# Optimization experiments

Measured on AMD Instinct MI355X. Metric: run time of the kernel, lower is better.

Reference implementation:

```python
import jax, jax.numpy as jnp
import numpy as np

EPS = 1e-06
FP8_MAX = 448.0  # float8_e4m3fn max
T, H = 8192, 4096


def setup_inputs() -> dict:
    key = jax.random.key(0)
    ks = jax.random.split(key, 5)
    return {
        "hidden_states": jax.random.normal(ks[0], (T, H), dtype=jnp.float32),
        "norm_w": jax.random.uniform(ks[1], (4, H), dtype=jnp.float32),
        "w": jax.random.uniform(ks[2], (3, H, H), dtype=jnp.float32),
        "wscale": jax.random.uniform(ks[3], (3,), dtype=jnp.float32),
        "scale": jax.random.uniform(ks[4], (3,), dtype=jnp.float32),
    }


def _rmsnorm(x, g):
    var = jnp.mean(x * x, axis=-1, keepdims=True)
    return x * jax.lax.rsqrt(var + EPS) * g


def _fp8_quant(x, s):
    # static per-tensor quant: scale, clamp to fp8 range, cast to e4m3 and back
    q = jnp.clip(x / s, -FP8_MAX, FP8_MAX)
    return q.astype(jnp.float8_e4m3fn).astype(jnp.float32)


def _fp8_linear(x, wq, s_in, s_w):
    qx = _fp8_quant(x, s_in)
    return (qx @ wq) * (s_in * s_w)


def reference(hidden_states, norm_w, w, wscale, scale):
    # weight fp8 quantization (module stores weights already in fp8)
    wq = w.astype(jnp.float8_e4m3fn).astype(jnp.float32)  # [3,H,H]

    z = jax.nn.relu(hidden_states)
    x = resid = z  # all_reduce == identity on one device
    y = _rmsnorm(x, norm_w[0])

    z2 = _fp8_linear(y, wq[0], scale[0], wscale[0])
    x2 = z2 + resid
    resid = x2
    y2 = _rmsnorm(x2, norm_w[1])

    z3 = _fp8_linear(y2, wq[1], scale[1], wscale[1])
    x3 = z3 + resid
    resid = x3
    y3 = _rmsnorm(x3, norm_w[2])

    z4 = _fp8_linear(y3, wq[2], scale[2], wscale[2])
    x4 = z4 + resid
    y4 = _rmsnorm(x4, norm_w[3])
    return y4
```

## Files before the change

### kernel.cpp

```cpp
#include <hip/hip_runtime.h>

typedef float f32x4  __attribute__((ext_vector_type(4)));
typedef float f32x16 __attribute__((ext_vector_type(16)));
typedef int   i32x4  __attribute__((ext_vector_type(4)));
typedef int   i32x8  __attribute__((ext_vector_type(8)));

#define T_DIM 8192
#define H_DIM 4096
#define SC1 0x7f7f7f7f

__device__ __forceinline__ unsigned int pack_fp8x4(float a, float b, float c, float d) {
    int v = __builtin_amdgcn_cvt_pk_fp8_f32(a, b, 0, false);
    v = __builtin_amdgcn_cvt_pk_fp8_f32(c, d, v, true);
    return (unsigned int)v;
}


__global__ __launch_bounds__(256) void wquant_kernel(
    const float* __restrict__ w, unsigned char* __restrict__ wqT)
{
    const int l  = blockIdx.z;
    const int n0 = blockIdx.x * 64;
    const int k0 = blockIdx.y * 64;
    const int tid = threadIdx.x;
    __shared__ unsigned char tile[64][68];
    const float* wl = w + (size_t)l * H_DIM * H_DIM;
#pragma unroll
    for (int p = 0; p < 4; ++p) {
        int r = p * 16 + (tid >> 4);
        int c = (tid & 15) * 4;
        f32x4 v = *(const f32x4*)(wl + (size_t)(k0 + r) * H_DIM + n0 + c);
        *(unsigned int*)&tile[r][c] = pack_fp8x4(v[0], v[1], v[2], v[3]);
    }
    __syncthreads();
    const int nl = tid >> 2;
    const int g  = tid & 3;
    unsigned int words[4];
#pragma unroll
    for (int wi = 0; wi < 4; ++wi) {
        unsigned int a = 0;
#pragma unroll
        for (int b = 0; b < 4; ++b)
            a |= (unsigned int)tile[g * 16 + wi * 4 + b][nl] << (8 * b);
        words[wi] = a;
    }
    const int bn = n0 >> 8, wc = (n0 >> 6) & 3, kt = k0 >> 6;
    const int n2 = nl >> 5;
    const int lane = (g >> 1) * 32 + (nl & 31);
    const int byte0 = (g & 1) * 16;
    const size_t off = ((((size_t)l * 16 + bn) * 64 + kt) * 4 + wc) * 2 + n2;
    unsigned char* op = wqT + off * 2048 + lane * 32 + byte0;
    uint4 ov; ov.x = words[0]; ov.y = words[1]; ov.z = words[2]; ov.w = words[3];
    *(uint4*)op = ov;
}

template <int MODE>
__global__ __launch_bounds__(256) void row_kernel(
    const float* __restrict__ in,
    float* __restrict__ resid_out,
    void* __restrict__ out,
    const float* __restrict__ g,
    const float* __restrict__ scale_p)
{
    const int row = blockIdx.x;
    const int tid = threadIdx.x;
    const float* rin = in + (size_t)row * H_DIM;
    float x[16];
    float ss = 0.0f;
#pragma unroll
    for (int j = 0; j < 4; ++j) {
        const int base = (j * 256 + tid) * 4;
        f32x4 v = *(const f32x4*)(rin + base);
        f32x4 rv;
#pragma unroll
        for (int i = 0; i < 4; ++i) {
            float t = v[i];
            if (MODE == 0) t = fmaxf(t, 0.0f);
            x[j * 4 + i] = t;
            rv[i] = t;
            ss += t * t;
        }
        if (MODE == 0)
            *(f32x4*)(resid_out + (size_t)row * H_DIM + base) = rv;
    }
#pragma unroll
    for (int off = 32; off > 0; off >>= 1)
        ss += __shfl_down(ss, off, 64);
    __shared__ float red[4];
    if ((tid & 63) == 0) red[tid >> 6] = ss;
    __syncthreads();
    const float var  = (red[0] + red[1] + red[2] + red[3]) * (1.0f / (float)H_DIM);
    const float rinv = 1.0f / sqrtf(var + 1e-6f);

    if (MODE == 2) {
        float* ro = (float*)out + (size_t)row * H_DIM;
#pragma unroll
        for (int j = 0; j < 4; ++j) {
            const int base = (j * 256 + tid) * 4;
            f32x4 gv = *(const f32x4*)(g + base);
            f32x4 ov;
#pragma unroll
            for (int i = 0; i < 4; ++i) ov[i] = (x[j * 4 + i] * rinv) * gv[i];
            *(f32x4*)(ro + base) = ov;
        }
    } else {
        const float s = scale_p[0];
        unsigned int* qo = (unsigned int*)out + (size_t)row * (H_DIM / 4);
#pragma unroll
        for (int j = 0; j < 4; ++j) {
            const int base = (j * 256 + tid) * 4;
            f32x4 gv = *(const f32x4*)(g + base);
            float q[4];
#pragma unroll
            for (int i = 0; i < 4; ++i) {
                float y = (x[j * 4 + i] * rinv) * gv[i];
                y = y / s;
                q[i] = fminf(fmaxf(y, -448.0f), 448.0f);
            }
            qo[j * 256 + tid] = pack_fp8x4(q[0], q[1], q[2], q[3]);
        }
    }
}

__device__ __forceinline__ void stage_half(const unsigned char* gsrc, unsigned char* ldsdst) {
    __builtin_amdgcn_global_load_lds(
        (const __attribute__((address_space(1))) unsigned int*)gsrc,
        (__attribute__((address_space(3))) unsigned int*)ldsdst, 16, 0, 0);
}

#define VM8 asm volatile("s_waitcnt vmcnt(8)" ::: "memory")
#define VM4 asm volatile("s_waitcnt vmcnt(4)" ::: "memory")
#define VM0 asm volatile("s_waitcnt vmcnt(0)" ::: "memory")
#define BAR __builtin_amdgcn_s_barrier()
#define PRIO1 __builtin_amdgcn_s_setprio(1)
#define PRIO0 __builtin_amdgcn_s_setprio(0)

#define MM2(m, S) do {                                                          \
    acc[m][0] = __builtin_amdgcn_mfma_scale_f32_32x32x64_f8f6f4(                \
        fa[m], b##S##0, acc[m][0], 0, 0, 0, SC1, 0, SC1);                       \
    acc[m][1] = __builtin_amdgcn_mfma_scale_f32_32x32x64_f8f6f4(                \
        fa[m], b##S##1, acc[m][1], 0, 0, 0, SC1, 0, SC1);                       \
} while (0)

#define RDA(BUF, m) do {                                                        \
    *(i32x4*)&fa[m]         = *(const i32x4*)(lds + (BUF) + wrA + (m) * 2048 + fo0); \
    *(((i32x4*)&fa[m]) + 1) = *(const i32x4*)(lds + (BUF) + wrA + (m) * 2048 + fo1); \
} while (0)

#define TILEBODY(S, BR) do {                                                    \
    PRIO1; MM2(0, S); PRIO0; RDA(BR, 0);                                        \
    PRIO1; MM2(1, S); PRIO0; RDA(BR, 1);                                        \
    PRIO1; MM2(2, S); PRIO0; RDA(BR, 2);                                        \
    PRIO1; MM2(3, S); PRIO0; RDA(BR, 3);                                        \
    __builtin_amdgcn_sched_group_barrier(0x008, 4, 0);                          \
    __builtin_amdgcn_sched_group_barrier(0x100, 4, 0);                          \
    __builtin_amdgcn_sched_group_barrier(0x008, 4, 0);                          \
    __builtin_amdgcn_sched_group_barrier(0x100, 4, 0);                          \
} while (0)

#define TILELAST(S) do {                                                        \
    PRIO1; MM2(0, S); MM2(1, S); MM2(2, S); MM2(3, S); PRIO0;                   \
} while (0)

#define LDB(NX) do {                                                            \
    bE##NX##0 = *(const i32x8*)(gB0 + kb);                                      \
    bE##NX##1 = *(const i32x8*)(gB0 + kb + 2048);                               \
    bO##NX##0 = *(const i32x8*)(gB0 + kb + 16384);                              \
    bO##NX##1 = *(const i32x8*)(gB0 + kb + 16384 + 2048);                       \
    kb += 32768;                                                                \
} while (0)

#define STG(KOFF, BUF) do {                                                     \
    stage_half(gAlo + (KOFF), lds + (BUF) + wave * 1024);                       \
    stage_half(gAhi + (KOFF), lds + (BUF) + 8192 + wave * 1024);                \
} while (0)

#define ITER(CU, NX, BR1, BR2, BS1, BS2) do {                                   \
    LDB(NX);                                                                    \
    STG(ka, BS1); STG(ka + 64, BS2); ka += 128;                                 \
    VM8; BAR;                                                                   \
    TILEBODY(E##CU, BR1);                                                       \
    TILEBODY(O##CU, BR2);                                                       \
} while (0)

__global__ __launch_bounds__(512, 2) void gemm_fp8_kernel(
    const unsigned char* __restrict__ A,
    const unsigned char* __restrict__ B,
    float* __restrict__ C,
    const float* __restrict__ s_in,
    const float* __restrict__ s_w)
{
    __shared__ unsigned char lds[98304];

    const float alpha = s_in[0] * s_w[0];

    const int b = blockIdx.x;
    const int local = b >> 3, chunk = b & 7;
    const int bm = (chunk & 3) * 8 + (local & 7);
    const int bn = (chunk >> 2) * 8 + (local >> 3);

    const int tid  = threadIdx.x;
    const int wave = tid >> 6;
    const int lane = tid & 63;
    const int wr   = wave >> 2;
    const int wc   = wave & 3;

    const int sw  = (lane >> 1) & 3;
    const int fo0 = (lane & 31) * 64 + ((((lane >> 5) * 2) + 0 ^ sw)) * 16;
    const int fo1 = (lane & 31) * 64 + ((((lane >> 5) * 2) + 1 ^ sw)) * 16;
    const int wrA = wr * 8192;

    const int voff = (tid >> 2) * H_DIM + ((tid & 3) ^ ((tid >> 3) & 3)) * 16;
    const unsigned char* gAlo = A + (size_t)bm * 256 * H_DIM + voff;
    const unsigned char* gAhi = gAlo + (size_t)128 * H_DIM;

    const unsigned char* gB0 =
        B + ((((size_t)bn * 64) * 4 + wc) * 2) * 2048 + lane * 32;

    f32x16 acc[4][2];
#pragma unroll
    for (int m = 0; m < 4; ++m)
#pragma unroll
        for (int n = 0; n < 2; ++n)
#pragma unroll
            for (int e = 0; e < 16; ++e) acc[m][n][e] = 0.0f;

    i32x8 fa[4];
    i32x8 bEA0, bEA1, bOA0, bOA1, bEB0, bEB1, bOB0, bOB1;
    int ka, kb;

    STG(0,   0);
    STG(64,  16384);
    STG(128, 32768);
    STG(192, 49152);
    kb = 0; LDB(A);
    VM0; BAR;
    RDA(0, 0); RDA(0, 1); RDA(0, 2); RDA(0, 3);
    ka = 256;

#pragma unroll 1
    for (int it = 0; it < 5; ++it) {
        ITER(A, B, 16384, 32768, 65536, 81920);
        ITER(B, A, 49152, 65536, 0,     16384);
        ITER(A, B, 81920, 0,     32768, 49152);
        ITER(B, A, 16384, 32768, 65536, 81920);
        ITER(A, B, 49152, 65536, 0,     16384);
        ITER(B, A, 81920, 0,     32768, 49152);
    }
    LDB(B);
    VM4; BAR;
    TILEBODY(EA, 16384);
    TILEBODY(OA, 32768);
    VM0; BAR;
    TILEBODY(EB, 49152);
    TILELAST(OB);

    const int lrow0 = bm * 256 + wr * 128 + 4 * (lane >> 5);
    const int lcol0 = bn * 256 + wc * 64 + (lane & 31);
#pragma unroll
    for (int m = 0; m < 4; ++m) {
#pragma unroll
        for (int n = 0; n < 2; ++n) {
#pragma unroll
            for (int e = 0; e < 16; ++e) {
                const int row = lrow0 + m * 32 + (e & 3) + 8 * (e >> 2);
                float* cp = C + (size_t)row * H_DIM + lcol0 + n * 32;
                *cp = acc[m][n][e] * alpha + *cp;
            }
        }
    }
}

extern "C" void kernel_launch(void* const* d_in, const int* in_sizes, int n_in,
                              void* d_out, int out_size, void* d_ws, size_t ws_size,
                              hipStream_t stream) {
    const float* h   = (const float*)d_in[0];
    const float* nw  = (const float*)d_in[1];
    const float* w   = (const float*)d_in[2];
    const float* wsc = (const float*)d_in[3];
    const float* sc  = (const float*)d_in[4];
    float* out = (float*)d_out;

    unsigned char* wqT = (unsigned char*)d_ws;
    unsigned char* qx  = wqT + (size_t)3 * H_DIM * H_DIM;
    float* resid = (float*)(qx + (size_t)T_DIM * H_DIM);

    const size_t WSTRIDE = (size_t)H_DIM * H_DIM;

    wquant_kernel<<<dim3(64, 64, 3), 256, 0, stream>>>(w, wqT);

    row_kernel<0><<<T_DIM, 256, 0, stream>>>(h, resid, qx, nw + 0 * H_DIM, sc + 0);
    gemm_fp8_kernel<<<512, 512, 0, stream>>>(qx, wqT + 0 * WSTRIDE, resid, sc + 0, wsc + 0);

    row_kernel<1><<<T_DIM, 256, 0, stream>>>(resid, nullptr, qx, nw + 1 * H_DIM, sc + 1);
    gemm_fp8_kernel<<<512, 512, 0, stream>>>(qx, wqT + 1 * WSTRIDE, resid, sc + 1, wsc + 1);

    row_kernel<1><<<T_DIM, 256, 0, stream>>>(resid, nullptr, qx, nw + 2 * H_DIM, sc + 2);
    gemm_fp8_kernel<<<512, 512, 0, stream>>>(qx, wqT + 2 * WSTRIDE, resid, sc + 2, wsc + 2);

    row_kernel<2><<<T_DIM, 256, 0, stream>>>(resid, nullptr, out, nw + 3 * H_DIM, nullptr);
}
```

Before: 754.9 us.

## Shrink GEMM block tile to 256x128 with triple-buffered LDS and more occupancy

Restructures the FP8 GEMM from a 256x256 block tile with 8 waves each holding a 128x64 sub-tile to a 256x128 block tile with 64x64 per wave. LDS drops from 96KB to 48KB with a three-buffer rotation, launch bounds allow 4 blocks per CU, and the grid doubles to 1024 blocks. The pipeline is rewritten to a single-stage prefetch per 64-wide K step with explicit lgkm/vm waits. The aim is more resident waves to hide latency and better load balance, at the cost of lower per-block data reuse (more A re-reads) and smaller MFMA batches per barrier.

```diff
diff --git a/kernel.cpp b/kernel.cpp
--- a/kernel.cpp
+++ b/kernel.cpp
@@ -128,18 +128,25 @@
         (__attribute__((address_space(3))) unsigned int*)ldsdst, 16, 0, 0);
 }
 
-#define VM8 asm volatile("s_waitcnt vmcnt(8)" ::: "memory")
+#define BUFA 0
+#define BUFB 16384
+#define BUFC 32768
+#define VM6 asm volatile("s_waitcnt vmcnt(6)" ::: "memory")
 #define VM4 asm volatile("s_waitcnt vmcnt(4)" ::: "memory")
-#define VM0 asm volatile("s_waitcnt vmcnt(0)" ::: "memory")
+#define LGKM0 asm volatile("s_waitcnt lgkmcnt(0)" ::: "memory")
 #define BAR __builtin_amdgcn_s_barrier()
 #define PRIO1 __builtin_amdgcn_s_setprio(1)
 #define PRIO0 __builtin_amdgcn_s_setprio(0)
 
-#define MM2(m, S) do {                                                          \
-    acc[m][0] = __builtin_amdgcn_mfma_scale_f32_32x32x64_f8f6f4(                \
-        fa[m], b##S##0, acc[m][0], 0, 0, 0, SC1, 0, SC1);                       \
-    acc[m][1] = __builtin_amdgcn_mfma_scale_f32_32x32x64_f8f6f4(                \
-        fa[m], b##S##1, acc[m][1], 0, 0, 0, SC1, 0, SC1);                       \
+#define MM4(P) do {                                                             \
+    acc[0][0] = __builtin_amdgcn_mfma_scale_f32_32x32x64_f8f6f4(                \
+        fa[0], b##P##0, acc[0][0], 0, 0, 0, SC1, 0, SC1);                       \
+    acc[0][1] = __builtin_amdgcn_mfma_scale_f32_32x32x64_f8f6f4(                \
+        fa[0], b##P##1, acc[0][1], 0, 0, 0, SC1, 0, SC1);                       \
+    acc[1][0] = __builtin_amdgcn_mfma_scale_f32_32x32x64_f8f6f4(                \
+        fa[1], b##P##0, acc[1][0], 0, 0, 0, SC1, 0, SC1);                       \
+    acc[1][1] = __builtin_amdgcn_mfma_scale_f32_32x32x64_f8f6f4(                \
+        fa[1], b##P##1, acc[1][1], 0, 0, 0, SC1, 0, SC1);                       \
 } while (0)
 
 #define RDA(BUF, m) do {                                                        \
@@ -147,118 +154,102 @@
     *(((i32x4*)&fa[m]) + 1) = *(const i32x4*)(lds + (BUF) + wrA + (m) * 2048 + fo1); \
 } while (0)
 
-#define TILEBODY(S, BR) do {                                                    \
-    PRIO1; MM2(0, S); PRIO0; RDA(BR, 0);                                        \
-    PRIO1; MM2(1, S); PRIO0; RDA(BR, 1);                                        \
-    PRIO1; MM2(2, S); PRIO0; RDA(BR, 2);                                        \
-    PRIO1; MM2(3, S); PRIO0; RDA(BR, 3);                                        \
-    __builtin_amdgcn_sched_group_barrier(0x008, 4, 0);                          \
-    __builtin_amdgcn_sched_group_barrier(0x100, 4, 0);                          \
-    __builtin_amdgcn_sched_group_barrier(0x008, 4, 0);                          \
-    __builtin_amdgcn_sched_group_barrier(0x100, 4, 0);                          \
-} while (0)
-
-#define TILELAST(S) do {                                                        \
-    PRIO1; MM2(0, S); MM2(1, S); MM2(2, S); MM2(3, S); PRIO0;                   \
-} while (0)
-
-#define LDB(NX) do {                                                            \
-    bE##NX##0 = *(const i32x8*)(gB0 + kb);                                      \
-    bE##NX##1 = *(const i32x8*)(gB0 + kb + 2048);                               \
-    bO##NX##0 = *(const i32x8*)(gB0 + kb + 16384);                              \
-    bO##NX##1 = *(const i32x8*)(gB0 + kb + 16384 + 2048);                       \
-    kb += 32768;                                                                \
-} while (0)
-
 #define STG(KOFF, BUF) do {                                                     \
     stage_half(gAlo + (KOFF), lds + (BUF) + wave * 1024);                       \
     stage_half(gAhi + (KOFF), lds + (BUF) + 8192 + wave * 1024);                \
 } while (0)
 
-#define ITER(CU, NX, BR1, BR2, BS1, BS2) do {                                   \
-    LDB(NX);                                                                    \
-    STG(ka, BS1); STG(ka + 64, BS2); ka += 128;                                 \
-    VM8; BAR;                                                                   \
-    TILEBODY(E##CU, BR1);                                                       \
-    TILEBODY(O##CU, BR2);                                                       \
-} while (0)
-
-__global__ __launch_bounds__(512, 2) void gemm_fp8_kernel(
+#define ITER(RB, WB, FC, FN) do {                                               \
+    BAR;                                                                        \
+    RDA(RB, 0); RDA(RB, 1);                                                     \
+    STG(ka, WB); ka += 64;                                                      \
+    b##FN##0 = *(const i32x8*)(gB0 + kb);                                       \
+    b##FN##1 = *(const i32x8*)(gB0 + kb + 2048);                                \
+    kb += 16384;                                                                \
+    PRIO1; MM4(FC); PRIO0;                                                      \
+    LGKM0; VM6;                                                                 \
+} while (0)
+
+__global__ __launch_bounds__(512, 4) void gemm_fp8_kernel(
     const unsigned char* __restrict__ A,
     const unsigned char* __restrict__ B,
     float* __restrict__ C,
     const float* __restrict__ s_in,
     const float* __restrict__ s_w)
 {
-    __shared__ unsigned char lds[98304];
+    __shared__ unsigned char lds[49152];
 
     const float alpha = s_in[0] * s_w[0];
 
     const int b = blockIdx.x;
-    const int local = b >> 3, chunk = b & 7;
-    const int bm = (chunk & 3) * 8 + (local & 7);
-    const int bn = (chunk >> 2) * 8 + (local >> 3);
+    const int chunk = b & 7, local = b >> 3;
+    const int bm = chunk * 4 + (local >> 5);
+    const int bn = local & 31;
 
     const int tid  = threadIdx.x;
     const int wave = tid >> 6;
     const int lane = tid & 63;
-    const int wr   = wave >> 2;
-    const int wc   = wave & 3;
+    const int wr   = wave >> 1;
+    const int wc   = wave & 1;
 
     const int sw  = (lane >> 1) & 3;
     const int fo0 = (lane & 31) * 64 + ((((lane >> 5) * 2) + 0 ^ sw)) * 16;
     const int fo1 = (lane & 31) * 64 + ((((lane >> 5) * 2) + 1 ^ sw)) * 16;
-    const int wrA = wr * 8192;
+    const int wrA = wr * 4096;
 
     const int voff = (tid >> 2) * H_DIM + ((tid & 3) ^ ((tid >> 3) & 3)) * 16;
     const unsigned char* gAlo = A + (size_t)bm * 256 * H_DIM + voff;
     const unsigned char* gAhi = gAlo + (size_t)128 * H_DIM;
 
+    const int cb = bn * 4 + wc * 2;
     const unsigned char* gB0 =
-        B + ((((size_t)bn * 64) * 4 + wc) * 2) * 2048 + lane * 32;
-
-    f32x16 acc[4][2];
-#pragma unroll
-    for (int m = 0; m < 4; ++m)
+        B + ((((size_t)(cb >> 3) * 64) * 4 + ((cb >> 1) & 3)) * 2 + (cb & 1)) * 2048
+          + lane * 32;
+
+    f32x16 acc[2][2];
+#pragma unroll
+    for (int m = 0; m < 2; ++m)
 #pragma unroll
         for (int n = 0; n < 2; ++n)
 #pragma unroll
             for (int e = 0; e < 16; ++e) acc[m][n][e] = 0.0f;
 
-    i32x8 fa[4];
-    i32x8 bEA0, bEA1, bOA0, bOA1, bEB0, bEB1, bOB0, bOB1;
-    int ka, kb;
-
-    STG(0,   0);
-    STG(64,  16384);
-    STG(128, 32768);
-    STG(192, 49152);
-    kb = 0; LDB(A);
-    VM0; BAR;
-    RDA(0, 0); RDA(0, 1); RDA(0, 2); RDA(0, 3);
-    ka = 256;
+    i32x8 fa[2];
+    i32x8 bE0, bE1, bO0, bO1;
+
+    STG(0,  BUFA);
+    STG(64, BUFB);
+    bE0 = *(const i32x8*)(gB0);
+    bE1 = *(const i32x8*)(gB0 + 2048);
+    VM4;
+    int ka = 128;
+    int kb = 16384;
 
 #pragma unroll 1
-    for (int it = 0; it < 5; ++it) {
-        ITER(A, B, 16384, 32768, 65536, 81920);
-        ITER(B, A, 49152, 65536, 0,     16384);
-        ITER(A, B, 81920, 0,     32768, 49152);
-        ITER(B, A, 16384, 32768, 65536, 81920);
-        ITER(A, B, 49152, 65536, 0,     16384);
-        ITER(B, A, 81920, 0,     32768, 49152);
-    }
-    LDB(B);
-    VM4; BAR;
-    TILEBODY(EA, 16384);
-    TILEBODY(OA, 32768);
-    VM0; BAR;
-    TILEBODY(EB, 49152);
-    TILELAST(OB);
-
-    const int lrow0 = bm * 256 + wr * 128 + 4 * (lane >> 5);
-    const int lcol0 = bn * 256 + wc * 64 + (lane & 31);
-#pragma unroll
-    for (int m = 0; m < 4; ++m) {
+    for (int it = 0; it < 10; ++it) {
+        ITER(BUFA, BUFC, E, O);
+        ITER(BUFB, BUFA, O, E);
+        ITER(BUFC, BUFB, E, O);
+        ITER(BUFA, BUFC, O, E);
+        ITER(BUFB, BUFA, E, O);
+        ITER(BUFC, BUFB, O, E);
+    }
+    ITER(BUFA, BUFC, E, O);
+    ITER(BUFB, BUFA, O, E);
+    BAR;
+    RDA(BUFC, 0); RDA(BUFC, 1);
+    bO0 = *(const i32x8*)(gB0 + kb);
+    bO1 = *(const i32x8*)(gB0 + kb + 2048);
+    PRIO1; MM4(E); PRIO0;
+    LGKM0; VM4;
+    BAR;
+    RDA(BUFA, 0); RDA(BUFA, 1);
+    PRIO1; MM4(O); PRIO0;
+
+    const int lrow0 = bm * 256 + wr * 64 + 4 * (lane >> 5);
+    const int lcol0 = bn * 128 + wc * 64 + (lane & 31);
+#pragma unroll
+    for (int m = 0; m < 2; ++m) {
 #pragma unroll
         for (int n = 0; n < 2; ++n) {
 #pragma unroll
@@ -290,13 +281,13 @@
     wquant_kernel<<<dim3(64, 64, 3), 256, 0, stream>>>(w, wqT);
 
     row_kernel<0><<<T_DIM, 256, 0, stream>>>(h, resid, qx, nw + 0 * H_DIM, sc + 0);
-    gemm_fp8_kernel<<<512, 512, 0, stream>>>(qx, wqT + 0 * WSTRIDE, resid, sc + 0, wsc + 0);
+    gemm_fp8_kernel<<<1024, 512, 0, stream>>>(qx, wqT + 0 * WSTRIDE, resid, sc + 0, wsc + 0);
 
     row_kernel<1><<<T_DIM, 256, 0, stream>>>(resid, nullptr, qx, nw + 1 * H_DIM, sc + 1);
-    gemm_fp8_kernel<<<512, 512, 0, stream>>>(qx, wqT + 1 * WSTRIDE, resid, sc + 1, wsc + 1);
+    gemm_fp8_kernel<<<1024, 512, 0, stream>>>(qx, wqT + 1 * WSTRIDE, resid, sc + 1, wsc + 1);
 
     row_kernel<1><<<T_DIM, 256, 0, stream>>>(resid, nullptr, qx, nw + 2 * H_DIM, sc + 2);
-    gemm_fp8_kernel<<<512, 512, 0, stream>>>(qx, wqT + 2 * WSTRIDE, resid, sc + 2, wsc + 2);
+    gemm_fp8_kernel<<<1024, 512, 0, stream>>>(qx, wqT + 2 * WSTRIDE, resid, sc + 2, wsc + 2);
 
     row_kernel<2><<<T_DIM, 256, 0, stream>>>(resid, nullptr, out, nw + 3 * H_DIM, nullptr);
 }
```

Result: faster. 712.7 us (-5.6%).
